# Performance work log

Hardware: AMD Instinct MI355X
Metric: run time of the kernel (lower is better)

The kernel has to match this reference:

```python
import jax, jax.numpy as jnp
import numpy as np

LEAF = 32
N = 262144          # num_nodes, power of 2
NLEV = 8            # HODLR levels
RANK = 16           # off-diagonal low-rank
NNZ = 1310720       # ~5 nnz per row


def setup_inputs() -> dict:
    key = jax.random.key(0)
    ks = jax.random.split(key, 24)
    inp = {}
    inp["leaf_blocks"] = jax.random.normal(ks[0], (1, N // LEAF, LEAF, LEAF), jnp.float32) * 0.1
    for l in range(NLEV):
        inp[f"u{l}"] = jax.random.normal(ks[1 + 2 * l], (1, N, RANK), jnp.float32) * 0.05
        inp[f"v{l}"] = jax.random.normal(ks[2 + 2 * l], (1, N, RANK), jnp.float32) * 0.05
    inp["A_indices"] = jax.random.randint(ks[17], (2, NNZ), 0, N, dtype=jnp.int32).astype(jnp.int64)
    inp["A_values"] = jax.random.normal(ks[18], (NNZ,), jnp.float32)
    inp["z"] = jax.random.normal(ks[19], (1, N, 1), jnp.float32)
    inp["num_nodes"] = N
    return inp


def apply_hodlr(leaf_blocks, factors, x, leaf_size=LEAF):
    # x: [B, n, 1]; leaf_blocks: [B, n/leaf, leaf, leaf]
    B, n, _ = x.shape
    nb = n // leaf_size
    xb = x.reshape(B, nb, leaf_size, 1)
    L = leaf_blocks
    # y = L @ (L^T @ x) + 1e-4 * x  per leaf block
    yb = jnp.matmul(L, jnp.matmul(jnp.swapaxes(L, -1, -2), xb)) + xb * 1e-4
    y = yb.reshape(B, n, 1)
    for li, (u, v) in enumerate(factors):
        num_splits = 2 ** (li + 1)
        bs = n // num_splits
        if bs == 0:
            continue
        npair = num_splits // 2
        vl = npair * 2 * bs  # == n for power-of-2 n
        xv = x[:, :vl].reshape(B, npair, 2, bs, 1)
        uv = u[:, :vl].reshape(B, npair, 2, bs, -1)
        vv = v[:, :vl].reshape(B, npair, 2, bs, -1)
        xL, xR = xv[:, :, 0], xv[:, :, 1]
        uL, uR = uv[:, :, 0], uv[:, :, 1]
        vL, vR = vv[:, :, 0], vv[:, :, 1]
        # cross-block low-rank updates: y_L += U_L (V_R^T x_R), y_R += U_R (V_L^T x_L)
        yL = jnp.matmul(uL, jnp.matmul(jnp.swapaxes(vR, -1, -2), xR))
        yR = jnp.matmul(uR, jnp.matmul(jnp.swapaxes(vL, -1, -2), xL))
        upd = jnp.stack([yL, yR], axis=2).reshape(B, vl, 1)
        if vl < n:
            upd = jnp.pad(upd, ((0, 0), (0, n - vl), (0, 0)))
        y = y + upd
    return y


def reference(leaf_blocks, u0, v0, u1, v1, u2, v2, u3, v3, u4, v4, u5, v5, u6, v6, u7, v7,
              A_indices, A_values, z, num_nodes):
    factors = [(u0, v0), (u1, v1), (u2, v2), (u3, v3),
               (u4, v4), (u5, v5), (u6, v6), (u7, v7)]
    w = apply_hodlr(leaf_blocks, factors, z)           # [1, N, 1]
    w_flat = w[0, :, 0]                                 # [N]
    rows, cols = A_indices[0], A_indices[1]
    # sparse COO matvec: y[r] = sum_k A_values[k] * w[cols[k]] over rows
    y_flat = jax.ops.segment_sum(A_values * w_flat[cols], rows, num_segments=num_nodes)
    y = y_flat.reshape(1, num_nodes, 1)
    return jnp.mean((y - z) ** 2)
```

## Files before the change

kernel.cpp:

```cpp
#include <hip/hip_runtime.h>

#define NN 262144
#define RANK 16
#define NNZ_K 1310720
#define NB 640
#define BPB 2048
#define NBKT 256
#define RPB 1024

struct P8 { const float* p[8]; };

__global__ __launch_bounds__(256) void k_levels_t(P8 v, const float* __restrict__ z,
                                                  float* __restrict__ part) {
    __shared__ float zl[512];
    __shared__ float red[8][4][16];
    const int tid  = threadIdx.x;
    const int base = blockIdx.x * 512;

    zl[tid]       = z[base + tid];
    zl[tid + 256] = z[base + tid + 256];
    __syncthreads();

    const int q = tid & 3;
    const int e = tid >> 2;

    float4 acc[8];
#pragma unroll
    for (int l = 0; l < 8; ++l) acc[l] = make_float4(0.f, 0.f, 0.f, 0.f);

#pragma unroll
    for (int it = 0; it < 8; ++it) {
        const int jloc = it * 64 + e;
        const size_t j = (size_t)(base + jloc);
        const float zz = zl[jloc];
#pragma unroll
        for (int l = 0; l < 8; ++l) {
            const float4 vv = *(const float4*)(v.p[l] + j * RANK + q * 4);
            acc[l].x += vv.x * zz;
            acc[l].y += vv.y * zz;
            acc[l].z += vv.z * zz;
            acc[l].w += vv.w * zz;
        }
    }

    const int lane = tid & 63;
    const int wv   = tid >> 6;
#pragma unroll
    for (int l = 0; l < 8; ++l) {
        float4 a = acc[l];
#pragma unroll
        for (int m = 4; m <= 32; m <<= 1) {
            a.x += __shfl_xor(a.x, m);
            a.y += __shfl_xor(a.y, m);
            a.z += __shfl_xor(a.z, m);
            a.w += __shfl_xor(a.w, m);
        }
        if (lane < 4) *(float4*)&red[l][wv][lane * 4] = a;
    }
    __syncthreads();

    if (tid < 128) {
        const int l = tid >> 4;
        const int r = tid & 15;
        const float s = red[l][0][r] + red[l][1][r] + red[l][2][r] + red[l][3][r];
        part[(l * 512 + blockIdx.x) * 16 + r] = s;
    }
}

__global__ __launch_bounds__(64) void k_reduce_t(const float* __restrict__ part,
                                                 float* __restrict__ tg,
                                                 float* __restrict__ loss) {
    const int b = blockIdx.x;
    if (b == 0 && threadIdx.x == 0) loss[0] = 0.f;
    const int t = b + 2;
    const int l = 30 - __clz(t);
    const int h = t - (2 << l);
    const int cnt = 256 >> l;
    const int c0  = h * cnt;
    const int r = threadIdx.x & 15;
    const int g = threadIdx.x >> 4;

    float s = 0.f;
    for (int c = c0 + g; c < c0 + cnt; c += 4)
        s += part[(l * 512 + c) * 16 + r];

    __shared__ float red[64];
    red[threadIdx.x] = s;
    __syncthreads();
    if (threadIdx.x < 16)
        tg[((2 << l) - 2 + h) * 16 + r] = red[r] + red[16 + r] + red[32 + r] + red[48 + r];
}

__global__ __launch_bounds__(256) void k_apply(const float* __restrict__ leaf, P8 u,
                                               const float* __restrict__ z,
                                               const float* __restrict__ tg,
                                               float* __restrict__ w,
                                               float* __restrict__ y) {
    __shared__ float Lp[8 * 1056];
    __shared__ float xl[256];
    __shared__ float t32[8][32];
    __shared__ float tl[8][16];

    const int tid  = threadIdx.x;
    const int base = blockIdx.x * 256;

    const float4* Lg = (const float4*)(leaf + (size_t)base * 32);
#pragma unroll
    for (int k = 0; k < 8; ++k) {
        const int fi = tid + k * 256;
        const float4 val = Lg[fi];
        const int lb  = fi >> 8;
        const int off = (fi & 255) * 4;
        const int row = off >> 5;
        const int col = off & 31;
        float* d = &Lp[lb * 1056 + row * 33 + col];
        d[0] = val.x; d[1] = val.y; d[2] = val.z; d[3] = val.w;
    }
    xl[tid] = z[base + tid];
    if (tid < 128) {
        const int l = tid >> 4;
        const int r = tid & 15;
        const int h = base >> (17 - l);
        tl[l][r] = tg[(((2 << l) - 2) + (h ^ 1)) * 16 + r];
    }
    __syncthreads();

    {
        const int lb = tid >> 5;
        const int c  = tid & 31;
        const float* Lb = &Lp[lb * 1056];
        const float* xb = &xl[lb * 32];
        float s = 0.f;
#pragma unroll
        for (int row = 0; row < 32; ++row)
            s += Lb[row * 33 + c] * xb[row];
        t32[lb][c] = s;
    }
    __syncthreads();

    {
        const int lb = tid >> 5;
        const int r  = tid & 31;
        const float* Lb = &Lp[lb * 1056 + r * 33];
        float acc = 1e-4f * xl[tid];
#pragma unroll
        for (int c = 0; c < 32; ++c)
            acc += Lb[c] * t32[lb][c];

        const size_t i = (size_t)(base + tid);
#pragma unroll
        for (int l = 0; l < 8; ++l) {
            const float4* up = (const float4*)(u.p[l] + i * RANK);
            const float4 a0 = up[0], a1 = up[1], a2 = up[2], a3 = up[3];
            acc += a0.x * tl[l][0]  + a0.y * tl[l][1]  + a0.z * tl[l][2]  + a0.w * tl[l][3]
                 + a1.x * tl[l][4]  + a1.y * tl[l][5]  + a1.z * tl[l][6]  + a1.w * tl[l][7]
                 + a2.x * tl[l][8]  + a2.y * tl[l][9]  + a2.z * tl[l][10] + a2.w * tl[l][11]
                 + a3.x * tl[l][12] + a3.y * tl[l][13] + a3.z * tl[l][14] + a3.w * tl[l][15];
        }
        w[i] = acc;
        if (y) y[i] = 0.f;
    }
}

__global__ __launch_bounds__(256) void k_bin(const int* __restrict__ idx,
                                             const float* __restrict__ vals,
                                             const float* __restrict__ w,
                                             unsigned long long* __restrict__ gpairs,
                                             int* __restrict__ gdesc) {
    __shared__ unsigned long long pairs[BPB];
    __shared__ int hist[NBKT];
    __shared__ int scan[NBKT];
    __shared__ int cursor[NBKT];

    const int t  = threadIdx.x;
    const int bl = blockIdx.x;
    const int base = bl * BPB;

    hist[t] = 0;
    __syncthreads();

    int   rows[8];
    float pv[8];
#pragma unroll
    for (int i = 0; i < 2; ++i) {
        const int k = base + i * 1024 + t * 4;
        const int4   r4 = *(const int4*)(idx + k);
        const int4   c4 = *(const int4*)(idx + NNZ_K + k);
        const float4 v4 = *(const float4*)(vals + k);
        rows[i*4+0] = r4.x; pv[i*4+0] = v4.x * w[c4.x];
        rows[i*4+1] = r4.y; pv[i*4+1] = v4.y * w[c4.y];
        rows[i*4+2] = r4.z; pv[i*4+2] = v4.z * w[c4.z];
        rows[i*4+3] = r4.w; pv[i*4+3] = v4.w * w[c4.w];
        atomicAdd(&hist[r4.x >> 10], 1);
        atomicAdd(&hist[r4.y >> 10], 1);
        atomicAdd(&hist[r4.z >> 10], 1);
        atomicAdd(&hist[r4.w >> 10], 1);
    }
    __syncthreads();

    const int cnt = hist[t];
    scan[t] = cnt;
    __syncthreads();
    for (int off = 1; off < NBKT; off <<= 1) {
        const int add = (t >= off) ? scan[t - off] : 0;
        __syncthreads();
        scan[t] += add;
        __syncthreads();
    }
    const int st = scan[t] - cnt;
    gdesc[t * NB + bl] = st | (cnt << 16);
    cursor[t] = st;
    __syncthreads();

#pragma unroll
    for (int i = 0; i < 8; ++i) {
        const int b   = rows[i] >> 10;
        const int pos = atomicAdd(&cursor[b], 1);
        pairs[pos] = ((unsigned long long)__float_as_uint(pv[i]) << 32) | (unsigned)rows[i];
    }
    __syncthreads();

    const ulonglong2* ps = (const ulonglong2*)pairs;
    ulonglong2*       pd = (ulonglong2*)(gpairs + (size_t)bl * BPB);
#pragma unroll
    for (int i = 0; i < 4; ++i)
        pd[i * 256 + t] = ps[i * 256 + t];
}

__global__ __launch_bounds__(512) void k_accum(const unsigned long long* __restrict__ gpairs,
                                               const int* __restrict__ gdesc,
                                               const float* __restrict__ z,
                                               float* __restrict__ loss) {
    __shared__ float acc[RPB];
    __shared__ float red[8];
    const int t = threadIdx.x;
    const int b = blockIdx.x;
    acc[t] = 0.f;
    acc[t + 512] = 0.f;
    __syncthreads();

    for (int bl = t; bl < NB; bl += 512) {
        const int d  = gdesc[b * NB + bl];
        const int st = d & 0xffff;
        const int c  = d >> 16;
        const unsigned long long* p = gpairs + (size_t)bl * BPB + st;
        for (int j = 0; j < c; ++j) {
            const unsigned long long pr = p[j];
            atomicAdd(&acc[(int)(pr & 1023u)], __uint_as_float((unsigned)(pr >> 32)));
        }
    }
    __syncthreads();

    float s = 0.f;
#pragma unroll
    for (int i = 0; i < 2; ++i) {
        const int r = i * 512 + t;
        const float d = acc[r] - z[b * RPB + r];
        s += d * d;
    }
#pragma unroll
    for (int m = 32; m >= 1; m >>= 1) s += __shfl_down(s, m);
    if ((t & 63) == 0) red[t >> 6] = s;
    __syncthreads();
    if (t == 0) {
        float tt = 0.f;
#pragma unroll
        for (int i = 0; i < 8; ++i) tt += red[i];
        atomicAdd(loss, tt);
    }
}

__global__ __launch_bounds__(256) void k_spmv(const int* __restrict__ idx,
                                              const float* __restrict__ vals,
                                              const float* __restrict__ w,
                                              float* __restrict__ y) {
    const int k = (blockIdx.x * 256 + threadIdx.x) * 4;
    const int4   r4 = *(const int4*)(idx + k);
    const int4   c4 = *(const int4*)(idx + NNZ_K + k);
    const float4 v4 = *(const float4*)(vals + k);
    atomicAdd(&y[r4.x], v4.x * w[c4.x]);
    atomicAdd(&y[r4.y], v4.y * w[c4.y]);
    atomicAdd(&y[r4.z], v4.z * w[c4.z]);
    atomicAdd(&y[r4.w], v4.w * w[c4.w]);
}

__global__ __launch_bounds__(256) void k_loss(const float* __restrict__ y,
                                              const float* __restrict__ z,
                                              float* __restrict__ loss) {
    const int i = blockIdx.x * 256 + threadIdx.x;
    const float4 a = ((const float4*)y)[i];
    const float4 b = ((const float4*)z)[i];
    const float dx = a.x - b.x, dy = a.y - b.y, dz = a.z - b.z, dw = a.w - b.w;
    float s = dx * dx + dy * dy + dz * dz + dw * dw;
#pragma unroll
    for (int m = 32; m >= 1; m >>= 1) s += __shfl_down(s, m);
    __shared__ float r4s[4];
    const int lane = threadIdx.x & 63, wv = threadIdx.x >> 6;
    if (lane == 0) r4s[wv] = s;
    __syncthreads();
    if (threadIdx.x == 0) atomicAdd(loss, r4s[0] + r4s[1] + r4s[2] + r4s[3]);
}

__global__ void k_fin(const float* __restrict__ loss, float* __restrict__ out) {
    out[0] = loss[0] * (1.0f / (float)NN);
}

extern "C" void kernel_launch(void* const* d_in, const int* in_sizes, int n_in,
                              void* d_out, int out_size, void* d_ws, size_t ws_size,
                              hipStream_t stream) {
    const float* leaf = (const float*)d_in[0];
    P8 u, v;
    for (int l = 0; l < 8; ++l) {
        u.p[l] = (const float*)d_in[1 + 2 * l];
        v.p[l] = (const float*)d_in[2 + 2 * l];
    }
    const int*   Aidx  = (const int*)d_in[17];
    const float* Avals = (const float*)d_in[18];
    const float* z     = (const float*)d_in[19];

    float* ws   = (float*)d_ws;
    float* part  = ws;
    float* tg    = ws + 65536;
    float* loss  = ws + 73728;
    float* w     = ws + 73792;
    int*   gdesc = (int*)(ws + 335936);
    unsigned long long* gpairs = (unsigned long long*)(ws + 499776);
    const size_t need_main = (size_t)(499776 + (size_t)NB * BPB * 2) * 4;

    k_levels_t<<<NN / 512, 256, 0, stream>>>(v, z, part);
    k_reduce_t<<<510, 64, 0, stream>>>(part, tg, loss);

    if (ws_size >= need_main) {
        k_apply<<<NN / 256, 256, 0, stream>>>(leaf, u, z, tg, w, nullptr);
        k_bin  <<<NB, 256, 0, stream>>>(Aidx, Avals, w, gpairs, gdesc);
        k_accum<<<NBKT, 512, 0, stream>>>(gpairs, gdesc, z, loss);
    } else {
        float* y = ws + 335936;
        k_apply<<<NN / 256, 256, 0, stream>>>(leaf, u, z, tg, w, y);
        k_spmv <<<NNZ_K / 1024, 256, 0, stream>>>(Aidx, Avals, w, y);
        k_loss <<<NN / 1024, 256, 0, stream>>>(y, z, loss);
    }
    k_fin<<<1, 1, 0, stream>>>(loss, (float*)d_out);
}
```

Baseline: 353.7 us.

## Split leaf-block apply from low-rank update stream and fold finalization into accumulation

```diff
diff --git a/kernel.cpp b/kernel.cpp
--- a/kernel.cpp
+++ b/kernel.cpp
@@ -71,7 +71,7 @@
                                                  float* __restrict__ tg,
                                                  float* __restrict__ loss) {
     const int b = blockIdx.x;
-    if (b == 0 && threadIdx.x == 0) loss[0] = 0.f;
+    if (b == 0 && threadIdx.x == 0) { loss[0] = 0.f; ((int*)loss)[1] = 0; }
     const int t = b + 2;
     const int l = 30 - __clz(t);
     const int h = t - (2 << l);
@@ -91,23 +91,20 @@
         tg[((2 << l) - 2 + h) * 16 + r] = red[r] + red[16 + r] + red[32 + r] + red[48 + r];
 }
 
-__global__ __launch_bounds__(256) void k_apply(const float* __restrict__ leaf, P8 u,
-                                               const float* __restrict__ z,
-                                               const float* __restrict__ tg,
-                                               float* __restrict__ w,
-                                               float* __restrict__ y) {
-    __shared__ float Lp[8 * 1056];
-    __shared__ float xl[256];
-    __shared__ float t32[8][32];
-    __shared__ float tl[8][16];
-
-    const int tid  = threadIdx.x;
-    const int base = blockIdx.x * 256;
+__global__ __launch_bounds__(128) void k_leaf(const float* __restrict__ leaf,
+                                              const float* __restrict__ z,
+                                              float* __restrict__ w) {
+    __shared__ float Lp[4 * 1056];
+    __shared__ float xl[128];
+    __shared__ float t32[4][32];
+
+    const int t    = threadIdx.x;
+    const int base = blockIdx.x * 128;
 
     const float4* Lg = (const float4*)(leaf + (size_t)base * 32);
 #pragma unroll
     for (int k = 0; k < 8; ++k) {
-        const int fi = tid + k * 256;
+        const int fi = t + k * 128;
         const float4 val = Lg[fi];
         const int lb  = fi >> 8;
         const int off = (fi & 255) * 4;
@@ -116,18 +113,12 @@
         float* d = &Lp[lb * 1056 + row * 33 + col];
         d[0] = val.x; d[1] = val.y; d[2] = val.z; d[3] = val.w;
     }
-    xl[tid] = z[base + tid];
-    if (tid < 128) {
-        const int l = tid >> 4;
-        const int r = tid & 15;
-        const int h = base >> (17 - l);
-        tl[l][r] = tg[(((2 << l) - 2) + (h ^ 1)) * 16 + r];
-    }
+    xl[t] = z[base + t];
     __syncthreads();
 
     {
-        const int lb = tid >> 5;
-        const int c  = tid & 31;
+        const int lb = t >> 5;
+        const int c  = t & 31;
         const float* Lb = &Lp[lb * 1056];
         const float* xb = &xl[lb * 32];
         float s = 0.f;
@@ -139,27 +130,42 @@
     __syncthreads();
 
     {
-        const int lb = tid >> 5;
-        const int r  = tid & 31;
-        const float* Lb = &Lp[lb * 1056 + r * 33];
-        float acc = 1e-4f * xl[tid];
+        const int lb = t >> 5;
+        const float* Lb = &Lp[lb * 1056 + (t & 31) * 33];
+        float acc = 1e-4f * xl[t];
 #pragma unroll
         for (int c = 0; c < 32; ++c)
             acc += Lb[c] * t32[lb][c];
-
-        const size_t i = (size_t)(base + tid);
-#pragma unroll
-        for (int l = 0; l < 8; ++l) {
-            const float4* up = (const float4*)(u.p[l] + i * RANK);
-            const float4 a0 = up[0], a1 = up[1], a2 = up[2], a3 = up[3];
-            acc += a0.x * tl[l][0]  + a0.y * tl[l][1]  + a0.z * tl[l][2]  + a0.w * tl[l][3]
-                 + a1.x * tl[l][4]  + a1.y * tl[l][5]  + a1.z * tl[l][6]  + a1.w * tl[l][7]
-                 + a2.x * tl[l][8]  + a2.y * tl[l][9]  + a2.z * tl[l][10] + a2.w * tl[l][11]
-                 + a3.x * tl[l][12] + a3.y * tl[l][13] + a3.z * tl[l][14] + a3.w * tl[l][15];
-        }
-        w[i] = acc;
-        if (y) y[i] = 0.f;
-    }
+        w[base + t] = acc;
+    }
+}
+
+__global__ __launch_bounds__(256) void k_ustream(P8 u, const float* __restrict__ tg,
+                                                 float* __restrict__ w) {
+    __shared__ float tl[8][16];
+    const int t    = threadIdx.x;
+    const int base = blockIdx.x * 256;
+
+    if (t < 128) {
+        const int l = t >> 4;
+        const int r = t & 15;
+        const int h = base >> (17 - l);
+        tl[l][r] = tg[(((2 << l) - 2) + (h ^ 1)) * 16 + r];
+    }
+    __syncthreads();
+
+    const size_t i = (size_t)(base + t);
+    float acc = w[i];
+#pragma unroll
+    for (int l = 0; l < 8; ++l) {
+        const float4* up = (const float4*)(u.p[l] + i * RANK);
+        const float4 a0 = up[0], a1 = up[1], a2 = up[2], a3 = up[3];
+        acc += a0.x * tl[l][0]  + a0.y * tl[l][1]  + a0.z * tl[l][2]  + a0.w * tl[l][3]
+             + a1.x * tl[l][4]  + a1.y * tl[l][5]  + a1.z * tl[l][6]  + a1.w * tl[l][7]
+             + a2.x * tl[l][8]  + a2.y * tl[l][9]  + a2.z * tl[l][10] + a2.w * tl[l][11]
+             + a3.x * tl[l][12] + a3.y * tl[l][13] + a3.z * tl[l][14] + a3.w * tl[l][15];
+    }
+    w[i] = acc;
 }
 
 __global__ __launch_bounds__(256) void k_bin(const int* __restrict__ idx,
@@ -230,7 +236,8 @@
 __global__ __launch_bounds__(512) void k_accum(const unsigned long long* __restrict__ gpairs,
                                                const int* __restrict__ gdesc,
                                                const float* __restrict__ z,
-                                               float* __restrict__ loss) {
+                                               float* __restrict__ loss,
+                                               float* __restrict__ out) {
     __shared__ float acc[RPB];
     __shared__ float red[8];
     const int t = threadIdx.x;
@@ -267,6 +274,12 @@
 #pragma unroll
         for (int i = 0; i < 8; ++i) tt += red[i];
         atomicAdd(loss, tt);
+        __threadfence();
+        const int old = atomicAdd((int*)loss + 1, 1);
+        if (old == NBKT - 1) {
+            __threadfence();
+            out[0] = loss[0] * (1.0f / (float)NN);
+        }
     }
 }
 
@@ -284,6 +297,10 @@
     atomicAdd(&y[r4.w], v4.w * w[c4.w]);
 }
 
+__global__ __launch_bounds__(256) void k_yzero(float* __restrict__ y) {
+    y[blockIdx.x * 256 + threadIdx.x] = 0.f;
+}
+
 __global__ __launch_bounds__(256) void k_loss(const float* __restrict__ y,
                                               const float* __restrict__ z,
                                               float* __restrict__ loss) {
@@ -327,18 +344,19 @@
     unsigned long long* gpairs = (unsigned long long*)(ws + 499776);
     const size_t need_main = (size_t)(499776 + (size_t)NB * BPB * 2) * 4;
 
+    k_leaf    <<<NN / 128, 128, 0, stream>>>(leaf, z, w);
     k_levels_t<<<NN / 512, 256, 0, stream>>>(v, z, part);
     k_reduce_t<<<510, 64, 0, stream>>>(part, tg, loss);
+    k_ustream <<<NN / 256, 256, 0, stream>>>(u, tg, w);
 
     if (ws_size >= need_main) {
-        k_apply<<<NN / 256, 256, 0, stream>>>(leaf, u, z, tg, w, nullptr);
         k_bin  <<<NB, 256, 0, stream>>>(Aidx, Avals, w, gpairs, gdesc);
-        k_accum<<<NBKT, 512, 0, stream>>>(gpairs, gdesc, z, loss);
+        k_accum<<<NBKT, 512, 0, stream>>>(gpairs, gdesc, z, loss, (float*)d_out);
     } else {
         float* y = ws + 335936;
-        k_apply<<<NN / 256, 256, 0, stream>>>(leaf, u, z, tg, w, y);
+        k_yzero<<<NN / 256, 256, 0, stream>>>(y);
         k_spmv <<<NNZ_K / 1024, 256, 0, stream>>>(Aidx, Avals, w, y);
         k_loss <<<NN / 1024, 256, 0, stream>>>(y, z, loss);
-    }
-    k_fin<<<1, 1, 0, stream>>>(loss, (float*)d_out);
-}
+        k_fin  <<<1, 1, 0, stream>>>(loss, (float*)d_out);
+    }
+}
```

Result: no change. 359.3 us (+1.6%).
